# Kernel optimization log

Measured on AMD Instinct MI355X. Metric: run time of the kernel, lower is better.

## Reference

```python
import jax, jax.numpy as jnp
import numpy as np

DIM = 1024
N_HEADS = 16
HEAD_DIM = DIM // N_HEADS
MAX_SEQ = 2048
BATCH = 4
SEQ = 2048


def _rope_tables(seq_len, head_dim):
    inv_freq = 1.0 / (10000.0 ** (jnp.arange(0, head_dim, 2, dtype=jnp.float32) / head_dim))
    t = jnp.arange(seq_len, dtype=jnp.float32)
    freqs = jnp.outer(t, inv_freq)            # [S, D/2]
    emb = jnp.concatenate([freqs, freqs], axis=-1)  # [S, D]
    return jnp.cos(emb), jnp.sin(emb)


def setup_inputs() -> dict:
    key = jax.random.key(0)
    kx, kq, kk, kv, ko = jax.random.split(key, 5)
    s = 1.0 / np.sqrt(DIM)
    x = jax.random.normal(kx, (BATCH, SEQ, DIM), dtype=jnp.float32)
    Wq = jax.random.normal(kq, (DIM, DIM), dtype=jnp.float32) * s
    Wk = jax.random.normal(kk, (DIM, DIM), dtype=jnp.float32) * s
    Wv = jax.random.normal(kv, (DIM, DIM), dtype=jnp.float32) * s
    Wo = jax.random.normal(ko, (DIM, DIM), dtype=jnp.float32) * s
    cos, sin = _rope_tables(SEQ, HEAD_DIM)
    mask = jnp.tril(jnp.ones((SEQ, SEQ), dtype=bool))[None, None]  # [1,1,S,S] causal
    return {"x": x, "Wq": Wq, "Wk": Wk, "Wv": Wv, "Wo": Wo,
            "cos": cos, "sin": sin, "mask": mask}


def _rotate_half(t):
    t1, t2 = jnp.split(t, 2, axis=-1)
    return jnp.concatenate([-t2, t1], axis=-1)


def reference(x, Wq, Wk, Wv, Wo, cos, sin, mask):
    B, S, _ = x.shape
    # projections (torch Linear: y = x @ W.T)
    q = (x @ Wq.T).reshape(B, S, N_HEADS, HEAD_DIM)
    k = (x @ Wk.T).reshape(B, S, N_HEADS, HEAD_DIM)
    v = (x @ Wv.T).reshape(B, S, N_HEADS, HEAD_DIM)
    # RoPE on [B,S,H,D]: cos/sin broadcast over batch and heads
    c = cos[None, :S, None, :]
    s_ = sin[None, :S, None, :]
    q = q * c + _rotate_half(q) * s_
    k = k * c + _rotate_half(k) * s_
    # attention, heads-major
    scale = HEAD_DIM ** -0.5
    attn = jnp.einsum('bqhd,bkhd->bhqk', q, k) * scale
    attn = jnp.where(mask, attn, -jnp.inf)
    attn = jax.nn.softmax(attn, axis=-1)
    out = jnp.einsum('bhqk,bkhd->bqhd', attn, v).reshape(B, S, DIM)
    return out @ Wo.T
```

## Files before the change

### kernel.cpp

```cpp
#include <hip/hip_runtime.h>
#include <hip/hip_bf16.h>
#include <stdint.h>

typedef __bf16 bf16;
typedef __bf16 bf16x8 __attribute__((ext_vector_type(8)));
typedef float f32x4 __attribute__((ext_vector_type(4)));

static constexpr int DIMM  = 1024;
static constexpr int NHEADS = 16;
static constexpr int HDIM  = 64;
static constexpr int SEQL  = 2048;
static constexpr int NB    = 4;
static constexpr int MTOT  = NB * SEQL;
static constexpr float LOG2E = 1.4426950408889634f;

__device__ __forceinline__ bool probe_fp32(const void* cosT) {
    return *(const uint32_t*)cosT != 0x3F803F80u;
}

__device__ __forceinline__ bf16x8 load8_any(const void* p, size_t off, bool f32) {
    if (f32) {
        const float* q = (const float*)p + off;
        f32x4 a = *(const f32x4*)q;
        f32x4 b = *(const f32x4*)(q + 4);
        bf16x8 r;
        r[0] = (bf16)a[0]; r[1] = (bf16)a[1]; r[2] = (bf16)a[2]; r[3] = (bf16)a[3];
        r[4] = (bf16)b[0]; r[5] = (bf16)b[1]; r[6] = (bf16)b[2]; r[7] = (bf16)b[3];
        return r;
    }
    return *(const bf16x8*)((const bf16*)p + off);
}

__device__ __forceinline__ float loadf_any(const void* p, size_t off, bool f32) {
    return f32 ? ((const float*)p)[off] : (float)((const bf16*)p)[off];
}

__device__ __forceinline__ int swz(int row, int kc) {
    return row * 128 + ((kc ^ (row & 7)) << 4);
}

__device__ __forceinline__ void gl_lds16(const bf16* g, bf16* l) {
    __builtin_amdgcn_global_load_lds(
        (const __attribute__((address_space(1))) unsigned int*)g,
        (__attribute__((address_space(3))) unsigned int*)l,
        16, 0, 0);
}

__global__ __launch_bounds__(256)
void cvt_kernel(const void* __restrict__ x,  const void* __restrict__ Wq,
                const void* __restrict__ Wk, const void* __restrict__ Wv,
                const void* __restrict__ Wo, const void* __restrict__ cosT,
                bf16* __restrict__ xb,  bf16* __restrict__ Wqb,
                bf16* __restrict__ Wkb, bf16* __restrict__ Wvb,
                bf16* __restrict__ Wob)
{
    const bool f32 = probe_fp32(cosT);
    const size_t NX = (size_t)MTOT * DIMM;
    const size_t NW = (size_t)DIMM * DIMM;
    size_t i = ((size_t)blockIdx.x * 256 + threadIdx.x) * 8;
    const void* src; bf16* dst; size_t off;
    if (i < NX) { src = x; dst = xb; off = i; }
    else {
        size_t j = i - NX;
        int wsel = (int)(j >> 20);
        off = j & (NW - 1);
        if      (wsel == 0) { src = Wq; dst = Wqb; }
        else if (wsel == 1) { src = Wk; dst = Wkb; }
        else if (wsel == 2) { src = Wv; dst = Wvb; }
        else                { src = Wo; dst = Wob; }
    }
    *(bf16x8*)(dst + off) = load8_any(src, off, f32);
}

template <class AAddr, class BAddr>
__device__ __forceinline__ void gemm_tile_gl(AAddr ga, BAddr gb,
                                             bf16* As, bf16* Bs, f32x4 acc[4][4])
{
    const int tid  = threadIdx.x;
    const int lane = tid & 63;
    const int w    = tid >> 6;
    const int l15  = lane & 15;
    const int lg   = lane >> 4;
    const int r8   = lane >> 3;
    const int c8   = lane & 7;
    const int wm   = (w >> 1) * 64;
    const int wn   = (w & 1) * 64;

    #pragma unroll
    for (int mf = 0; mf < 4; ++mf)
        #pragma unroll
        for (int nf = 0; nf < 4; ++nf)
            acc[mf][nf] = f32x4{0.f, 0.f, 0.f, 0.f};

    for (int kt = 0; kt < DIMM / 64; ++kt) {
        const int k0 = kt * 64;
        #pragma unroll
        for (int i = 0; i < 4; ++i) {
            const int c   = w * 4 + i;
            const int row = c * 8 + r8;
            gl_lds16(ga(row, k0 + c8 * 8), As + c * 512);
            gl_lds16(gb(row, k0 + c8 * 8), Bs + c * 512);
        }
        __syncthreads();
        #pragma unroll
        for (int ks = 0; ks < 2; ++ks) {
            bf16x8 af[4], bfr[4];
            #pragma unroll
            for (int mf = 0; mf < 4; ++mf)
                af[mf] = *(const bf16x8*)(As + (wm + mf * 16 + l15) * 64 + (ks * 4 + lg) * 8);
            #pragma unroll
            for (int nf = 0; nf < 4; ++nf)
                bfr[nf] = *(const bf16x8*)(Bs + (wn + nf * 16 + l15) * 64 + (ks * 4 + lg) * 8);
            #pragma unroll
            for (int mf = 0; mf < 4; ++mf)
                #pragma unroll
                for (int nf = 0; nf < 4; ++nf)
                    acc[mf][nf] = __builtin_amdgcn_mfma_f32_16x16x32_bf16(
                        af[mf], bfr[nf], acc[mf][nf], 0, 0, 0);
        }
        __syncthreads();
    }
}

__global__ __launch_bounds__(256, 2)
void qkv_kernel(const bf16* __restrict__ xb,
                const bf16* __restrict__ Wqb, const bf16* __restrict__ Wkb,
                const bf16* __restrict__ Wvb,
                const void* __restrict__ cosT, const void* __restrict__ sinT,
                bf16* __restrict__ qb, bf16* __restrict__ kb, bf16* __restrict__ vTb)
{
    __shared__ __align__(16) bf16 As[128 * 64];
    __shared__ __align__(16) bf16 Bs[3][128 * 64];

    const bool f32 = probe_fp32(cosT);
    const int bm = (int)blockIdx.x * 128;
    const int bn = (int)blockIdx.y * 128;

    const int tid  = threadIdx.x;
    const int lane = tid & 63;
    const int w    = tid >> 6;
    const int l15  = lane & 15;
    const int lg   = lane >> 4;
    const int r8   = lane >> 3;
    const int c8   = lane & 7;
    const int wm   = (w >> 1) * 64;
    const int wn   = (w & 1) * 64;

    f32x4 acc[3][4][4];
    #pragma unroll
    for (int w3 = 0; w3 < 3; ++w3)
        #pragma unroll
        for (int mf = 0; mf < 4; ++mf)
            #pragma unroll
            for (int nf = 0; nf < 4; ++nf)
                acc[w3][mf][nf] = f32x4{0.f, 0.f, 0.f, 0.f};

    const int kcs = (c8 ^ r8) * 8;

    for (int kt = 0; kt < DIMM / 64; ++kt) {
        const int k0 = kt * 64;
        #pragma unroll
        for (int i = 0; i < 4; ++i) {
            const int c   = w * 4 + i;
            const int row = c * 8 + r8;
            gl_lds16(xb  + (size_t)(bm + row) * DIMM + k0 + kcs, As    + c * 512);
            gl_lds16(Wqb + (size_t)(bn + row) * DIMM + k0 + kcs, Bs[0] + c * 512);
            gl_lds16(Wkb + (size_t)(bn + row) * DIMM + k0 + kcs, Bs[1] + c * 512);
            gl_lds16(Wvb + (size_t)(bn + row) * DIMM + k0 + kcs, Bs[2] + c * 512);
        }
        __syncthreads();
        #pragma unroll
        for (int ks = 0; ks < 2; ++ks) {
            bf16x8 af[4];
            #pragma unroll
            for (int mf = 0; mf < 4; ++mf)
                af[mf] = *(const bf16x8*)((const char*)As + swz(wm + mf * 16 + l15, ks * 4 + lg));
            #pragma unroll
            for (int w3 = 0; w3 < 3; ++w3) {
                bf16x8 bfr[4];
                #pragma unroll
                for (int nf = 0; nf < 4; ++nf)
                    bfr[nf] = *(const bf16x8*)((const char*)Bs[w3] + swz(wn + nf * 16 + l15, ks * 4 + lg));
                #pragma unroll
                for (int mf = 0; mf < 4; ++mf)
                    #pragma unroll
                    for (int nf = 0; nf < 4; ++nf)
                        acc[w3][mf][nf] = __builtin_amdgcn_mfma_f32_16x16x32_bf16(
                            af[mf], bfr[nf], acc[w3][mf][nf], 0, 0, 0);
            }
        }
        __syncthreads();
    }

    #pragma unroll
    for (int mf = 0; mf < 4; ++mf) {
        #pragma unroll
        for (int nf = 0; nf < 4; ++nf) {
            int n = bn + wn + nf * 16 + l15;
            int h = n >> 6;
            int d = n & 63;
            float sign = (d < 32) ? -1.f : 1.f;
            #pragma unroll
            for (int r = 0; r < 4; ++r) {
                int m = bm + wm + mf * 16 + lg * 4 + r;
                int b = m >> 11, s = m & 2047;
                float c  = loadf_any(cosT, s * 64 + d, f32);
                float sv = loadf_any(sinT, s * 64 + d, f32);
                size_t o_qk = ((size_t)((b * NHEADS + h) * SEQL + s)) * HDIM + d;
                float q0 = acc[0][mf][nf][r], q1 = acc[0][mf][nf ^ 2][r];
                float k0v = acc[1][mf][nf][r], k1 = acc[1][mf][nf ^ 2][r];
                qb[o_qk] = (bf16)((q0 * c + sign * q1 * sv) * 0.125f);
                kb[o_qk] = (bf16)(k0v * c + sign * k1 * sv);
                vTb[((size_t)((b * NHEADS + h) * HDIM + d)) * SEQL + s] = (bf16)acc[2][mf][nf][r];
            }
        }
    }
}

__global__ __launch_bounds__(256, 3)
void attn_kernel(bf16* __restrict__ qb, const bf16* __restrict__ kb,
                 const bf16* __restrict__ vTb)
{
    __shared__ __align__(16) bf16 Ks[2][64 * 64];
    __shared__ __align__(16) bf16 Vs[2][64 * 64];
    __shared__ __align__(16) bf16 Pl[4][32 * 64];

    const int bh  = blockIdx.x;
    const int qt  = 15 - (int)blockIdx.y;
    const int tid = threadIdx.x;
    const int lane = tid & 63, w = tid >> 6;
    const int l15 = lane & 15, lg = lane >> 4;

    bf16*       Qp = qb  + (size_t)bh * SEQL * HDIM;
    const bf16* Kp = kb  + (size_t)bh * SEQL * HDIM;
    const bf16* Vp = vTb + (size_t)bh * HDIM * SEQL;

    const int q0  = qt * 128 + w * 32;
    const int njt = 2 * qt + 2;

    bf16x8 qf[2][2];
    #pragma unroll
    for (int mi = 0; mi < 2; ++mi)
        #pragma unroll
        for (int ks = 0; ks < 2; ++ks)
            qf[mi][ks] = *(const bf16x8*)(Qp + (size_t)(q0 + mi * 16 + l15) * HDIM + ks * 32 + lg * 8);

    bf16x8 ones;
    #pragma unroll
    for (int e = 0; e < 8; ++e) ones[e] = (bf16)1.0f;

    f32x4 oacc[2][4];
    f32x4 lacc[2];
    #pragma unroll
    for (int mi = 0; mi < 2; ++mi) {
        lacc[mi] = f32x4{0.f, 0.f, 0.f, 0.f};
        #pragma unroll
        for (int nd = 0; nd < 4; ++nd) oacc[mi][nd] = f32x4{0.f, 0.f, 0.f, 0.f};
    }

    char* Pw = (char*)Pl[w];
    const int srow0 = tid >> 3;
    const int skc   = tid & 7;

    bf16x8 kr[2], vr[2];
    auto issue = [&](int j) {
        const int kk0 = j * 64;
        #pragma unroll
        for (int c = 0; c < 2; ++c) {
            int row = c * 32 + srow0;
            kr[c] = *(const bf16x8*)(Kp + (size_t)(kk0 + row) * HDIM + skc * 8);
            vr[c] = *(const bf16x8*)(Vp + (size_t)row * SEQL + kk0 + skc * 8);
        }
    };
    auto commit = [&](int b) {
        #pragma unroll
        for (int c = 0; c < 2; ++c) {
            int row = c * 32 + srow0;
            *(bf16x8*)((char*)Ks[b] + swz(row, skc)) = kr[c];
            *(bf16x8*)((char*)Vs[b] + swz(row, skc)) = vr[c];
        }
    };

    issue(0);
    commit(0);
    __syncthreads();

    for (int j = 0; j < njt; ++j) {
        const int kk0 = j * 64;
        const int buf = j & 1;
        const bool more = (j + 1 < njt);
        if (more) issue(j + 1);

        f32x4 sacc[2][4];
        #pragma unroll
        for (int mi = 0; mi < 2; ++mi)
            #pragma unroll
            for (int nf = 0; nf < 4; ++nf)
                sacc[mi][nf] = f32x4{0.f, 0.f, 0.f, 0.f};
        #pragma unroll
        for (int ks = 0; ks < 2; ++ks) {
            bf16x8 kf[4];
            #pragma unroll
            for (int nf = 0; nf < 4; ++nf)
                kf[nf] = *(const bf16x8*)((const char*)Ks[buf] + swz(nf * 16 + l15, ks * 4 + lg));
            #pragma unroll
            for (int mi = 0; mi < 2; ++mi)
                #pragma unroll
                for (int nf = 0; nf < 4; ++nf)
                    sacc[mi][nf] = __builtin_amdgcn_mfma_f32_16x16x32_bf16(
                        qf[mi][ks], kf[nf], sacc[mi][nf], 0, 0, 0);
        }

        const bool nm = (kk0 + 63 > q0);
        #pragma unroll
        for (int mi = 0; mi < 2; ++mi)
            #pragma unroll
            for (int nf = 0; nf < 4; ++nf)
                #pragma unroll
                for (int r = 0; r < 4; ++r) {
                    float s = sacc[mi][nf][r];
                    if (nm) {
                        int kkk = kk0 + nf * 16 + l15;
                        int qq  = q0 + mi * 16 + lg * 4 + r;
                        if (kkk > qq) s = -1.0e30f;
                    }
                    float p = exp2f(s * LOG2E);
                    int row = mi * 16 + lg * 4 + r;
                    int col = nf * 16 + l15;
                    *(bf16*)(Pw + row * 128 + ((col * 2) ^ ((row & 7) << 4))) = (bf16)p;
                }

        #pragma unroll
        for (int ks = 0; ks < 2; ++ks) {
            bf16x8 pf[2], vf[4];
            #pragma unroll
            for (int mi = 0; mi < 2; ++mi)
                pf[mi] = *(const bf16x8*)(Pw + swz(mi * 16 + l15, ks * 4 + lg));
            #pragma unroll
            for (int nd = 0; nd < 4; ++nd)
                vf[nd] = *(const bf16x8*)((const char*)Vs[buf] + swz(nd * 16 + l15, ks * 4 + lg));
            #pragma unroll
            for (int mi = 0; mi < 2; ++mi)
                lacc[mi] = __builtin_amdgcn_mfma_f32_16x16x32_bf16(
                    pf[mi], ones, lacc[mi], 0, 0, 0);
            #pragma unroll
            for (int mi = 0; mi < 2; ++mi)
                #pragma unroll
                for (int nd = 0; nd < 4; ++nd)
                    oacc[mi][nd] = __builtin_amdgcn_mfma_f32_16x16x32_bf16(
                        pf[mi], vf[nd], oacc[mi][nd], 0, 0, 0);
        }

        if (more) {
            commit(buf ^ 1);
            __syncthreads();
        }
    }

    #pragma unroll
    for (int mi = 0; mi < 2; ++mi)
        #pragma unroll
        for (int nd = 0; nd < 4; ++nd)
            #pragma unroll
            for (int r = 0; r < 4; ++r) {
                int s = q0 + mi * 16 + lg * 4 + r;
                int d = nd * 16 + l15;
                float o = oacc[mi][nd][r] / lacc[mi][r];
                Qp[(size_t)s * HDIM + d] = (bf16)o;
            }
}

__global__ __launch_bounds__(256)
void oproj_kernel(const bf16* __restrict__ O, const bf16* __restrict__ Wob,
                  const void* __restrict__ cosT, void* __restrict__ outp)
{
    __shared__ __align__(16) bf16 As[128 * 64];
    __shared__ __align__(16) bf16 Bs[128 * 64];
    const bool f32 = probe_fp32(cosT);
    const int bm = blockIdx.x * 128;
    const int bn = blockIdx.y * 128;

    f32x4 acc[4][4];
    gemm_tile_gl(
        [&](int row, int k) {
            int m = bm + row;
            int b = m >> 11, s = m & 2047;
            int h = k >> 6, dd = k & 63;
            return O + ((size_t)((b * NHEADS + h) * SEQL + s)) * HDIM + dd;
        },
        [&](int row, int k) { return Wob + (size_t)(bn + row) * DIMM + k; },
        As, Bs, acc);

    const int tid = threadIdx.x;
    const int lane = tid & 63, wid = tid >> 6;
    const int l15 = lane & 15, lg = lane >> 4;
    const int wm = (wid >> 1) * 64, wn = (wid & 1) * 64;

    #pragma unroll
    for (int mf = 0; mf < 4; ++mf)
        #pragma unroll
        for (int nf = 0; nf < 4; ++nf) {
            int n = bn + wn + nf * 16 + l15;
            #pragma unroll
            for (int r = 0; r < 4; ++r) {
                int m = bm + wm + mf * 16 + lg * 4 + r;
                float v = acc[mf][nf][r];
                if (f32) ((float*)outp)[(size_t)m * DIMM + n] = v;
                else     ((bf16*)outp)[(size_t)m * DIMM + n] = (bf16)v;
            }
        }
}

extern "C" void kernel_launch(void* const* d_in, const int* in_sizes, int n_in,
                              void* d_out, int out_size, void* d_ws, size_t ws_size,
                              hipStream_t stream)
{
    const void* x    = d_in[0];
    const void* Wq   = d_in[1];
    const void* Wk   = d_in[2];
    const void* Wv   = d_in[3];
    const void* Wo   = d_in[4];
    const void* cosT = d_in[5];
    const void* sinT = d_in[6];

    const size_t NELEM = (size_t)MTOT * DIMM;
    const size_t NW    = (size_t)DIMM * DIMM;
    bf16* qb  = (bf16*)d_ws;
    bf16* kb  = qb + NELEM;
    bf16* vT  = kb + NELEM;
    bf16* xb  = vT + NELEM;
    bf16* Wqb = xb + NELEM;
    bf16* Wkb = Wqb + NW;
    bf16* Wvb = Wkb + NW;
    bf16* Wob = Wvb + NW;

    dim3 blk(256);
    cvt_kernel<<<dim3(6144), blk, 0, stream>>>(x, Wq, Wk, Wv, Wo, cosT,
                                               xb, Wqb, Wkb, Wvb, Wob);

    dim3 g1(MTOT / 128, DIMM / 128);
    qkv_kernel<<<g1, blk, 0, stream>>>(xb, Wqb, Wkb, Wvb, cosT, sinT, qb, kb, vT);

    dim3 g2(NB * NHEADS, SEQL / 128);
    attn_kernel<<<g2, blk, 0, stream>>>(qb, kb, vT);

    dim3 g3(MTOT / 128, DIMM / 128);
    oproj_kernel<<<g3, blk, 0, stream>>>(qb, Wob, cosT, d_out);
}
```

Baseline: 216.8 us.

## Transpose attention MFMAs so each lane owns a query row, drop ones-MFMA rowsum

The attention kernel now computes S^T and O^T by swapping MFMA operands, so each lane holds the scores for a single query row. This lets the row sum be accumulated in registers with two cross-lane shuffles at the end, replacing the extra MFMA against a vector of ones. P and O are stored as packed 4-element vectors instead of scalar bf16 writes. log2(e) is folded into the Q scaling in the projection kernel, removing one multiply per score. The row sum now comes from fp32 probabilities rather than bf16-rounded ones, which slightly changes the numerics.

Result: faster. 183.4 us (-15.4%).

```diff
diff --git a/kernel.cpp b/kernel.cpp
--- a/kernel.cpp
+++ b/kernel.cpp
@@ -3,6 +3,7 @@
 #include <stdint.h>
 
 typedef __bf16 bf16;
+typedef __bf16 bf16x4 __attribute__((ext_vector_type(4)));
 typedef __bf16 bf16x8 __attribute__((ext_vector_type(8)));
 typedef float f32x4 __attribute__((ext_vector_type(4)));
 
@@ -209,7 +210,7 @@
                 size_t o_qk = ((size_t)((b * NHEADS + h) * SEQL + s)) * HDIM + d;
                 float q0 = acc[0][mf][nf][r], q1 = acc[0][mf][nf ^ 2][r];
                 float k0v = acc[1][mf][nf][r], k1 = acc[1][mf][nf ^ 2][r];
-                qb[o_qk] = (bf16)((q0 * c + sign * q1 * sv) * 0.125f);
+                qb[o_qk] = (bf16)((q0 * c + sign * q1 * sv) * (0.125f * LOG2E));
                 kb[o_qk] = (bf16)(k0v * c + sign * k1 * sv);
                 vTb[((size_t)((b * NHEADS + h) * HDIM + d)) * SEQL + s] = (bf16)acc[2][mf][nf][r];
             }
@@ -240,25 +241,21 @@
 
     bf16x8 qf[2][2];
     #pragma unroll
-    for (int mi = 0; mi < 2; ++mi)
+    for (int mf = 0; mf < 2; ++mf)
         #pragma unroll
         for (int ks = 0; ks < 2; ++ks)
-            qf[mi][ks] = *(const bf16x8*)(Qp + (size_t)(q0 + mi * 16 + l15) * HDIM + ks * 32 + lg * 8);
-
-    bf16x8 ones;
-    #pragma unroll
-    for (int e = 0; e < 8; ++e) ones[e] = (bf16)1.0f;
-
-    f32x4 oacc[2][4];
-    f32x4 lacc[2];
-    #pragma unroll
-    for (int mi = 0; mi < 2; ++mi) {
-        lacc[mi] = f32x4{0.f, 0.f, 0.f, 0.f};
-        #pragma unroll
-        for (int nd = 0; nd < 4; ++nd) oacc[mi][nd] = f32x4{0.f, 0.f, 0.f, 0.f};
-    }
+            qf[mf][ks] = *(const bf16x8*)(Qp + (size_t)(q0 + mf * 16 + l15) * HDIM + ks * 32 + lg * 8);
+
+    f32x4 oacc[4][2];
+    float lsum[2] = {0.f, 0.f};
+    #pragma unroll
+    for (int nd = 0; nd < 4; ++nd)
+        #pragma unroll
+        for (int mf = 0; mf < 2; ++mf)
+            oacc[nd][mf] = f32x4{0.f, 0.f, 0.f, 0.f};
 
     char* Pw = (char*)Pl[w];
+    const int l7 = l15 & 7;
     const int srow0 = tid >> 3;
     const int skc   = tid & 7;
 
@@ -291,12 +288,12 @@
         const bool more = (j + 1 < njt);
         if (more) issue(j + 1);
 
-        f32x4 sacc[2][4];
-        #pragma unroll
-        for (int mi = 0; mi < 2; ++mi)
-            #pragma unroll
-            for (int nf = 0; nf < 4; ++nf)
-                sacc[mi][nf] = f32x4{0.f, 0.f, 0.f, 0.f};
+        f32x4 sacc[4][2];
+        #pragma unroll
+        for (int nf = 0; nf < 4; ++nf)
+            #pragma unroll
+            for (int mf = 0; mf < 2; ++mf)
+                sacc[nf][mf] = f32x4{0.f, 0.f, 0.f, 0.f};
         #pragma unroll
         for (int ks = 0; ks < 2; ++ks) {
             bf16x8 kf[4];
@@ -304,51 +301,54 @@
             for (int nf = 0; nf < 4; ++nf)
                 kf[nf] = *(const bf16x8*)((const char*)Ks[buf] + swz(nf * 16 + l15, ks * 4 + lg));
             #pragma unroll
-            for (int mi = 0; mi < 2; ++mi)
-                #pragma unroll
-                for (int nf = 0; nf < 4; ++nf)
-                    sacc[mi][nf] = __builtin_amdgcn_mfma_f32_16x16x32_bf16(
-                        qf[mi][ks], kf[nf], sacc[mi][nf], 0, 0, 0);
+            for (int nf = 0; nf < 4; ++nf)
+                #pragma unroll
+                for (int mf = 0; mf < 2; ++mf)
+                    sacc[nf][mf] = __builtin_amdgcn_mfma_f32_16x16x32_bf16(
+                        kf[nf], qf[mf][ks], sacc[nf][mf], 0, 0, 0);
         }
 
         const bool nm = (kk0 + 63 > q0);
         #pragma unroll
-        for (int mi = 0; mi < 2; ++mi)
-            #pragma unroll
-            for (int nf = 0; nf < 4; ++nf)
+        for (int nf = 0; nf < 4; ++nf) {
+            #pragma unroll
+            for (int mf = 0; mf < 2; ++mf) {
+                float pv[4];
                 #pragma unroll
                 for (int r = 0; r < 4; ++r) {
-                    float s = sacc[mi][nf][r];
+                    float s = sacc[nf][mf][r];
                     if (nm) {
-                        int kkk = kk0 + nf * 16 + l15;
-                        int qq  = q0 + mi * 16 + lg * 4 + r;
-                        if (kkk > qq) s = -1.0e30f;
+                        int kv = kk0 + nf * 16 + lg * 4 + r;
+                        int qq = q0 + mf * 16 + l15;
+                        if (kv > qq) s = -1.0e30f;
                     }
-                    float p = exp2f(s * LOG2E);
-                    int row = mi * 16 + lg * 4 + r;
-                    int col = nf * 16 + l15;
-                    *(bf16*)(Pw + row * 128 + ((col * 2) ^ ((row & 7) << 4))) = (bf16)p;
+                    pv[r] = exp2f(s);
                 }
+                lsum[mf] += (pv[0] + pv[1]) + (pv[2] + pv[3]);
+                bf16x4 pb;
+                pb[0] = (bf16)pv[0]; pb[1] = (bf16)pv[1];
+                pb[2] = (bf16)pv[2]; pb[3] = (bf16)pv[3];
+                *(bf16x4*)(Pw + (mf * 16 + l15) * 128
+                              + (((2 * nf + (lg >> 1)) ^ l7) << 4) + (lg & 1) * 8) = pb;
+            }
+        }
 
         #pragma unroll
         for (int ks = 0; ks < 2; ++ks) {
             bf16x8 pf[2], vf[4];
             #pragma unroll
-            for (int mi = 0; mi < 2; ++mi)
-                pf[mi] = *(const bf16x8*)(Pw + swz(mi * 16 + l15, ks * 4 + lg));
+            for (int mf = 0; mf < 2; ++mf)
+                pf[mf] = *(const bf16x8*)(Pw + (mf * 16 + l15) * 128
+                                             + (((ks * 4 + lg) ^ l7) << 4));
             #pragma unroll
             for (int nd = 0; nd < 4; ++nd)
                 vf[nd] = *(const bf16x8*)((const char*)Vs[buf] + swz(nd * 16 + l15, ks * 4 + lg));
             #pragma unroll
-            for (int mi = 0; mi < 2; ++mi)
-                lacc[mi] = __builtin_amdgcn_mfma_f32_16x16x32_bf16(
-                    pf[mi], ones, lacc[mi], 0, 0, 0);
-            #pragma unroll
-            for (int mi = 0; mi < 2; ++mi)
-                #pragma unroll
-                for (int nd = 0; nd < 4; ++nd)
-                    oacc[mi][nd] = __builtin_amdgcn_mfma_f32_16x16x32_bf16(
-                        pf[mi], vf[nd], oacc[mi][nd], 0, 0, 0);
+            for (int nd = 0; nd < 4; ++nd)
+                #pragma unroll
+                for (int mf = 0; mf < 2; ++mf)
+                    oacc[nd][mf] = __builtin_amdgcn_mfma_f32_16x16x32_bf16(
+                        vf[nd], pf[mf], oacc[nd][mf], 0, 0, 0);
         }
 
         if (more) {
@@ -358,16 +358,23 @@
     }
 
     #pragma unroll
-    for (int mi = 0; mi < 2; ++mi)
-        #pragma unroll
-        for (int nd = 0; nd < 4; ++nd)
-            #pragma unroll
-            for (int r = 0; r < 4; ++r) {
-                int s = q0 + mi * 16 + lg * 4 + r;
-                int d = nd * 16 + l15;
-                float o = oacc[mi][nd][r] / lacc[mi][r];
-                Qp[(size_t)s * HDIM + d] = (bf16)o;
-            }
+    for (int mf = 0; mf < 2; ++mf) {
+        lsum[mf] += __shfl_xor(lsum[mf], 16);
+        lsum[mf] += __shfl_xor(lsum[mf], 32);
+    }
+    float inv[2] = {1.f / lsum[0], 1.f / lsum[1]};
+    #pragma unroll
+    for (int nd = 0; nd < 4; ++nd)
+        #pragma unroll
+        for (int mf = 0; mf < 2; ++mf) {
+            bf16x4 o4;
+            #pragma unroll
+            for (int r = 0; r < 4; ++r)
+                o4[r] = (bf16)(oacc[nd][mf][r] * inv[mf]);
+            int s = q0 + mf * 16 + l15;
+            int d = nd * 16 + lg * 4;
+            *(bf16x4*)(Qp + (size_t)s * HDIM + d) = o4;
+        }
 }
 
 __global__ __launch_bounds__(256)
```
